# Performance work log

Hardware: AMD Instinct MI355X
Metric: run time of the kernel (lower is better)

Reference implementation:

```python
import jax, jax.numpy as jnp
import numpy as np

N_NODES = 100000
N_EDGES = 640000
D = 128

def setup_inputs() -> dict:
    key = jax.random.key(0)
    k1, k2, k3 = jax.random.split(key, 3)
    z = jax.random.normal(k1, (N_NODES, D), dtype=jnp.float32)
    edge_index = jax.random.randint(k2, (2, N_EDGES), 0, N_NODES, dtype=jnp.int64)
    # torch.nn.Bilinear(D, D, 1): weight (1, D, D), bias (1,); kaiming-like init, here random
    W = jax.random.normal(k3, (D, D), dtype=jnp.float32) * (1.0 / np.sqrt(D))
    b = jnp.zeros((1,), dtype=jnp.float32)
    return {"z": z, "edge_index": edge_index, "W": W, "b": b}

def reference(z, edge_index, W, b):
    # y_e = z[src_e]^T W z[dst_e] + b
    zi = z[edge_index[0]]            # [E, D] gather
    zj = z[edge_index[1]]            # [E, D] gather
    # (zi @ W) * zj summed over feature dim -> [E]
    y = jnp.einsum('ed,ed->e', zi @ W, zj) + b[0]
    return y
```

## Files before the change

### kernel.cpp

```cpp
#include <hip/hip_runtime.h>

#define FD 128

typedef __attribute__((ext_vector_type(8))) short short8;
typedef __attribute__((ext_vector_type(4))) float f32x4;

__device__ __forceinline__ unsigned short f2bf(float f) {
    unsigned u = __float_as_uint(f);
    u += 0x7fff + ((u >> 16) & 1);
    return (unsigned short)(u >> 16);
}
__device__ __forceinline__ float bf2f(unsigned short h) {
    return __uint_as_float(((unsigned)h) << 16);
}
__device__ __forceinline__ int bdot4(unsigned x, unsigned y, int acc) {
#if __has_builtin(__builtin_amdgcn_sdot4)
    return __builtin_amdgcn_sdot4(x, y, acc, false);
#else
    acc += (((int)(x << 24)) >> 24) * (((int)(y << 24)) >> 24);
    acc += (((int)(x << 16)) >> 24) * (((int)(y << 16)) >> 24);
    acc += (((int)(x <<  8)) >> 24) * (((int)(y <<  8)) >> 24);
    acc += (((int)x) >> 24)         * (((int)y) >> 24);
    return acc;
#endif
}
__device__ __forceinline__ unsigned pack4f(float a, float b, float c, float d, float inv) {
    const int q0 = (int)rintf(a * inv), q1 = (int)rintf(b * inv);
    const int q2 = (int)rintf(c * inv), q3 = (int)rintf(d * inv);
    return (unsigned)(q0 & 255) | ((unsigned)(q1 & 255) << 8) |
           ((unsigned)(q2 & 255) << 16) | ((unsigned)(q3 & 255) << 24);
}

__global__ void wt_kernel(const float* __restrict__ W, unsigned short* __restrict__ Wt) {
    const int tid = blockIdx.x * 256 + (int)threadIdx.x;
    const int n  = tid & 127;
    const int k0 = (tid >> 7) * 8;
    short8 w;
    #pragma unroll
    for (int j = 0; j < 8; ++j) w[j] = (short)f2bf(W[(k0 + j) * FD + n]);
    *(short8*)(Wt + (size_t)n * FD + k0) = w;
}

__global__ __launch_bounds__(256)
void u_mfma8(const float* __restrict__ z, const unsigned short* __restrict__ Wt,
             unsigned char* __restrict__ u8, float* __restrict__ uscale,
             unsigned char* __restrict__ z8, float* __restrict__ zscale,
             int nrows) {
    __shared__ unsigned short Wl[FD * FD];
    char* ldsb = (char*)Wl;
    const int tid  = (int)threadIdx.x;
    const int lane = tid & 63;
    const int wave = tid >> 6;
    const int l16  = lane & 15;
    const int kq   = lane >> 4;

    const long rowbase = (long)blockIdx.x * 64 + wave * 16;
    const long r  = rowbase + l16;
    const long rc = (r < nrows) ? r : (long)(nrows - 1);
    const bool rok = (r < nrows);

    float4 zf[4][2];
    #pragma unroll
    for (int ks = 0; ks < 4; ++ks) {
        const float4* zp = (const float4*)(z + rc * FD + kq * 32 + ks * 8);
        zf[ks][0] = zp[0];
        zf[ks][1] = zp[1];
    }

    #pragma unroll
    for (int i = 0; i < 8; ++i) {
        const int c = i * 256 + tid;
        const int n = c >> 4;
        const int o = (c & 15) * 16;
        short8 v = *(const short8*)(Wt + (size_t)n * FD + (c & 15) * 8);
        *(short8*)(ldsb + n * 256 + (o ^ ((n & 7) << 4))) = v;
    }
    __syncthreads();

    f32x4 acc[8];
    #pragma unroll
    for (int nt = 0; nt < 8; ++nt)
        acc[nt] = (f32x4){0.f, 0.f, 0.f, 0.f};

    short8 avk[4];
    float zmax = 1e-30f;

    #pragma unroll
    for (int ks = 0; ks < 4; ++ks) {
        const float4 f0 = zf[ks][0];
        const float4 f1 = zf[ks][1];
        short8 av;
        av[0] = (short)f2bf(f0.x); av[1] = (short)f2bf(f0.y);
        av[2] = (short)f2bf(f0.z); av[3] = (short)f2bf(f0.w);
        av[4] = (short)f2bf(f1.x); av[5] = (short)f2bf(f1.y);
        av[6] = (short)f2bf(f1.z); av[7] = (short)f2bf(f1.w);
        avk[ks] = av;
        #pragma unroll
        for (int j = 0; j < 8; ++j)
            zmax = fmaxf(zmax, fabsf(bf2f((unsigned short)av[j])));

        #pragma unroll
        for (int nt = 0; nt < 8; ++nt) {
            const int row = nt * 16 + l16;
            const short8 a = *(const short8*)(
                ldsb + row * 256 + ((kq * 64 + ks * 16) ^ ((row & 7) << 4)));
            acc[nt] = __builtin_amdgcn_mfma_f32_16x16x32_bf16(a, av, acc[nt], 0, 0, 0);
        }
    }

    zmax = fmaxf(zmax, __shfl_xor(zmax, 16, 64));
    zmax = fmaxf(zmax, __shfl_xor(zmax, 32, 64));
    {
        const float inv = 127.0f / zmax;
        uint4 p0, p1;
        p0.x = pack4f(bf2f((unsigned short)avk[0][0]), bf2f((unsigned short)avk[0][1]),
                      bf2f((unsigned short)avk[0][2]), bf2f((unsigned short)avk[0][3]), inv);
        p0.y = pack4f(bf2f((unsigned short)avk[0][4]), bf2f((unsigned short)avk[0][5]),
                      bf2f((unsigned short)avk[0][6]), bf2f((unsigned short)avk[0][7]), inv);
        p0.z = pack4f(bf2f((unsigned short)avk[1][0]), bf2f((unsigned short)avk[1][1]),
                      bf2f((unsigned short)avk[1][2]), bf2f((unsigned short)avk[1][3]), inv);
        p0.w = pack4f(bf2f((unsigned short)avk[1][4]), bf2f((unsigned short)avk[1][5]),
                      bf2f((unsigned short)avk[1][6]), bf2f((unsigned short)avk[1][7]), inv);
        p1.x = pack4f(bf2f((unsigned short)avk[2][0]), bf2f((unsigned short)avk[2][1]),
                      bf2f((unsigned short)avk[2][2]), bf2f((unsigned short)avk[2][3]), inv);
        p1.y = pack4f(bf2f((unsigned short)avk[2][4]), bf2f((unsigned short)avk[2][5]),
                      bf2f((unsigned short)avk[2][6]), bf2f((unsigned short)avk[2][7]), inv);
        p1.z = pack4f(bf2f((unsigned short)avk[3][0]), bf2f((unsigned short)avk[3][1]),
                      bf2f((unsigned short)avk[3][2]), bf2f((unsigned short)avk[3][3]), inv);
        p1.w = pack4f(bf2f((unsigned short)avk[3][4]), bf2f((unsigned short)avk[3][5]),
                      bf2f((unsigned short)avk[3][6]), bf2f((unsigned short)avk[3][7]), inv);
        if (rok) {
            *(uint4*)(z8 + r * FD + kq * 32)      = p0;
            *(uint4*)(z8 + r * FD + kq * 32 + 16) = p1;
            if (kq == 0) zscale[r] = zmax * (1.0f / 127.0f);
        }
    }

    float umax = 1e-30f;
    #pragma unroll
    for (int nt = 0; nt < 8; ++nt) {
        const f32x4 v = acc[nt];
        umax = fmaxf(umax, fmaxf(fmaxf(fabsf(v[0]), fabsf(v[1])),
                                 fmaxf(fabsf(v[2]), fabsf(v[3]))));
    }
    umax = fmaxf(umax, __shfl_xor(umax, 16, 64));
    umax = fmaxf(umax, __shfl_xor(umax, 32, 64));
    umax = fmaxf(umax, 1e-30f);
    const float uinv = 127.0f / umax;
    if (rok) {
        #pragma unroll
        for (int nt = 0; nt < 8; ++nt) {
            const f32x4 v = acc[nt];
            *(unsigned*)(u8 + r * FD + nt * 16 + kq * 4) =
                pack4f(v[0], v[1], v[2], v[3], uinv);
        }
        if (kq == 0) uscale[r] = umax * (1.0f / 127.0f);
    }
}

__global__ __launch_bounds__(256)
void edge8p2(const unsigned char* __restrict__ u8, const unsigned char* __restrict__ z8,
             const float* __restrict__ uscale, const float* __restrict__ zscale,
             const int* __restrict__ src, const int* __restrict__ dst,
             const float* __restrict__ bias, float* __restrict__ out, int E) {
    const int tid  = (int)threadIdx.x;
    const int lane = tid & 63;
    const int sub  = lane >> 3;
    const int l8   = lane & 7;
    const long wv  = (long)blockIdx.x * 4 + (tid >> 6);
    const long S   = (long)gridDim.x * 4 * 8;
    const float bv = bias[0];
    const long Em1 = (long)E - 1;

    long e = wv * 8 + sub;
    long ec  = (e     < E) ? e     : Em1;
    long ecn = (e + S < E) ? e + S : Em1;
    int s0 = src[ec],  t0 = dst[ec];
    int s1 = src[ecn], t1 = dst[ecn];
    uint4 xu0 = *((const uint4*)(u8 + (size_t)s0 * FD) + l8);
    uint4 xz0 = *((const uint4*)(z8 + (size_t)t0 * FD) + l8);
    float su0 = uscale[s0], sz0 = zscale[t0];

    while (e < E) {
        const uint4 xu1 = *((const uint4*)(u8 + (size_t)s1 * FD) + l8);
        const uint4 xz1 = *((const uint4*)(z8 + (size_t)t1 * FD) + l8);
        const float su1 = uscale[s1], sz1 = zscale[t1];

        const long e2  = e + 2 * S;
        const long e2c = (e2 < E) ? e2 : Em1;
        const int s2 = src[e2c], t2 = dst[e2c];

        int sum = 0;
        sum = bdot4(xu0.x, xz0.x, sum);
        sum = bdot4(xu0.y, xz0.y, sum);
        sum = bdot4(xu0.z, xz0.z, sum);
        sum = bdot4(xu0.w, xz0.w, sum);
        sum += __shfl_xor(sum, 4, 64);
        sum += __shfl_xor(sum, 2, 64);
        sum += __shfl_xor(sum, 1, 64);
        if (l8 == 0) out[e] = (float)sum * su0 * sz0 + bv;

        e += S;
        xu0 = xu1; xz0 = xz1; su0 = su1; sz0 = sz1;
        s1 = s2; t1 = t2;
    }
}

__global__ __launch_bounds__(128)
void bilinear_fused_fallback(const float* __restrict__ z, const float* __restrict__ Wg,
                             const int* __restrict__ src, const int* __restrict__ dst,
                             const float* __restrict__ bias, float* __restrict__ out,
                             int E) {
    __shared__ float Wl[FD * FD];
    __shared__ float zs[FD];
    __shared__ float red[2];
    for (int i = threadIdx.x; i < FD * FD; i += 128) Wl[i] = Wg[i];
    __syncthreads();
    const int j = (int)threadIdx.x;
    for (int e = blockIdx.x; e < E; e += gridDim.x) {
        const int s = src[e];
        const int t = dst[e];
        zs[j] = z[(size_t)s * FD + j];
        __syncthreads();
        float acc = 0.f;
        #pragma unroll 8
        for (int d = 0; d < FD; ++d) acc += zs[d] * Wl[d * FD + j];
        float p = acc * z[(size_t)t * FD + j];
        #pragma unroll
        for (int off = 32; off >= 1; off >>= 1)
            p += __shfl_xor(p, off, 64);
        if ((j & 63) == 0) red[j >> 6] = p;
        __syncthreads();
        if (j == 0) out[e] = red[0] + red[1] + bias[0];
        __syncthreads();
    }
}

extern "C" void kernel_launch(void* const* d_in, const int* in_sizes, int n_in,
                              void* d_out, int out_size, void* d_ws, size_t ws_size,
                              hipStream_t stream) {
    const float* z    = (const float*)d_in[0];
    const int*   ei   = (const int*)d_in[1];
    const float* W    = (const float*)d_in[2];
    const float* bias = (const float*)d_in[3];
    float* out = (float*)d_out;

    const int nrows = in_sizes[0] / FD;
    const int E     = in_sizes[1] / 2;
    const int* src = ei;
    const int* dst = ei + E;

    const size_t sz8 = (size_t)nrows * FD;
    const size_t szs = (size_t)nrows * sizeof(float);
    const size_t need = 2 * sz8 + 2 * szs + 256;

    if (ws_size >= need) {
        char* wsp = (char*)d_ws;
        unsigned char* u8  = (unsigned char*)wsp;
        unsigned char* z8  = (unsigned char*)(wsp + sz8);
        float* uscale = (float*)(wsp + 2 * sz8);
        float* zscale = (float*)(wsp + 2 * sz8 + szs);
        unsigned short* Wt = (unsigned short*)d_out;

        wt_kernel<<<8, 256, 0, stream>>>(W, Wt);
        const int nb1 = (nrows + 63) / 64;
        u_mfma8<<<nb1, 256, 0, stream>>>(z, Wt, u8, uscale, z8, zscale, nrows);
        edge8p2<<<2048, 256, 0, stream>>>(u8, z8, uscale, zscale, src, dst, bias, out, E);
    } else {
        bilinear_fused_fallback<<<2048, 128, 0, stream>>>(z, W, src, dst, bias, out, E);
    }
}
```

Before: 56.35 us.

## Make node projection kernel persistent with software-prefetched z tiles

Converts the per-node u = zW projection kernel from one block per 64-row tile into a persistent grid of at most 768 blocks that loop over tiles. W is staged into LDS once per block instead of once per tile, and the next tile's z rows are prefetched into registers while the current tile's MFMA work and quantization run. This trades some register pressure and reduced parallelism for fewer redundant W loads and overlap of global reads with compute.

New measurement: 56.56 us. No clear change (+0.4%).

```diff
diff --git a/kernel.cpp b/kernel.cpp
--- a/kernel.cpp
+++ b/kernel.cpp
@@ -42,10 +42,10 @@
 }
 
 __global__ __launch_bounds__(256)
-void u_mfma8(const float* __restrict__ z, const unsigned short* __restrict__ Wt,
+void u_mfma9(const float* __restrict__ z, const unsigned short* __restrict__ Wt,
              unsigned char* __restrict__ u8, float* __restrict__ uscale,
              unsigned char* __restrict__ z8, float* __restrict__ zscale,
-             int nrows) {
+             int nrows, int ntiles) {
     __shared__ unsigned short Wl[FD * FD];
     char* ldsb = (char*)Wl;
     const int tid  = (int)threadIdx.x;
@@ -53,18 +53,19 @@
     const int wave = tid >> 6;
     const int l16  = lane & 15;
     const int kq   = lane >> 4;
-
-    const long rowbase = (long)blockIdx.x * 64 + wave * 16;
-    const long r  = rowbase + l16;
-    const long rc = (r < nrows) ? r : (long)(nrows - 1);
-    const bool rok = (r < nrows);
-
+    const long NB  = gridDim.x;
+
+    long tile = blockIdx.x;
     float4 zf[4][2];
-    #pragma unroll
-    for (int ks = 0; ks < 4; ++ks) {
-        const float4* zp = (const float4*)(z + rc * FD + kq * 32 + ks * 8);
-        zf[ks][0] = zp[0];
-        zf[ks][1] = zp[1];
+    if (tile < ntiles) {
+        const long r0  = tile * 64 + wave * 16 + l16;
+        const long rc0 = (r0 < nrows) ? r0 : (long)(nrows - 1);
+        #pragma unroll
+        for (int ks = 0; ks < 4; ++ks) {
+            const float4* zp = (const float4*)(z + rc0 * FD + kq * 32 + ks * 8);
+            zf[ks][0] = zp[0];
+            zf[ks][1] = zp[1];
+        }
     }
 
     #pragma unroll
@@ -77,84 +78,102 @@
     }
     __syncthreads();
 
-    f32x4 acc[8];
-    #pragma unroll
-    for (int nt = 0; nt < 8; ++nt)
-        acc[nt] = (f32x4){0.f, 0.f, 0.f, 0.f};
-
-    short8 avk[4];
-    float zmax = 1e-30f;
-
-    #pragma unroll
-    for (int ks = 0; ks < 4; ++ks) {
-        const float4 f0 = zf[ks][0];
-        const float4 f1 = zf[ks][1];
-        short8 av;
-        av[0] = (short)f2bf(f0.x); av[1] = (short)f2bf(f0.y);
-        av[2] = (short)f2bf(f0.z); av[3] = (short)f2bf(f0.w);
-        av[4] = (short)f2bf(f1.x); av[5] = (short)f2bf(f1.y);
-        av[6] = (short)f2bf(f1.z); av[7] = (short)f2bf(f1.w);
-        avk[ks] = av;
-        #pragma unroll
-        for (int j = 0; j < 8; ++j)
-            zmax = fmaxf(zmax, fabsf(bf2f((unsigned short)av[j])));
-
-        #pragma unroll
-        for (int nt = 0; nt < 8; ++nt) {
-            const int row = nt * 16 + l16;
-            const short8 a = *(const short8*)(
-                ldsb + row * 256 + ((kq * 64 + ks * 16) ^ ((row & 7) << 4)));
-            acc[nt] = __builtin_amdgcn_mfma_f32_16x16x32_bf16(a, av, acc[nt], 0, 0, 0);
-        }
-    }
-
-    zmax = fmaxf(zmax, __shfl_xor(zmax, 16, 64));
-    zmax = fmaxf(zmax, __shfl_xor(zmax, 32, 64));
-    {
-        const float inv = 127.0f / zmax;
-        uint4 p0, p1;
-        p0.x = pack4f(bf2f((unsigned short)avk[0][0]), bf2f((unsigned short)avk[0][1]),
-                      bf2f((unsigned short)avk[0][2]), bf2f((unsigned short)avk[0][3]), inv);
-        p0.y = pack4f(bf2f((unsigned short)avk[0][4]), bf2f((unsigned short)avk[0][5]),
-                      bf2f((unsigned short)avk[0][6]), bf2f((unsigned short)avk[0][7]), inv);
-        p0.z = pack4f(bf2f((unsigned short)avk[1][0]), bf2f((unsigned short)avk[1][1]),
-                      bf2f((unsigned short)avk[1][2]), bf2f((unsigned short)avk[1][3]), inv);
-        p0.w = pack4f(bf2f((unsigned short)avk[1][4]), bf2f((unsigned short)avk[1][5]),
-                      bf2f((unsigned short)avk[1][6]), bf2f((unsigned short)avk[1][7]), inv);
-        p1.x = pack4f(bf2f((unsigned short)avk[2][0]), bf2f((unsigned short)avk[2][1]),
-                      bf2f((unsigned short)avk[2][2]), bf2f((unsigned short)avk[2][3]), inv);
-        p1.y = pack4f(bf2f((unsigned short)avk[2][4]), bf2f((unsigned short)avk[2][5]),
-                      bf2f((unsigned short)avk[2][6]), bf2f((unsigned short)avk[2][7]), inv);
-        p1.z = pack4f(bf2f((unsigned short)avk[3][0]), bf2f((unsigned short)avk[3][1]),
-                      bf2f((unsigned short)avk[3][2]), bf2f((unsigned short)avk[3][3]), inv);
-        p1.w = pack4f(bf2f((unsigned short)avk[3][4]), bf2f((unsigned short)avk[3][5]),
-                      bf2f((unsigned short)avk[3][6]), bf2f((unsigned short)avk[3][7]), inv);
-        if (rok) {
-            *(uint4*)(z8 + r * FD + kq * 32)      = p0;
-            *(uint4*)(z8 + r * FD + kq * 32 + 16) = p1;
-            if (kq == 0) zscale[r] = zmax * (1.0f / 127.0f);
-        }
-    }
-
-    float umax = 1e-30f;
-    #pragma unroll
-    for (int nt = 0; nt < 8; ++nt) {
-        const f32x4 v = acc[nt];
-        umax = fmaxf(umax, fmaxf(fmaxf(fabsf(v[0]), fabsf(v[1])),
-                                 fmaxf(fabsf(v[2]), fabsf(v[3]))));
-    }
-    umax = fmaxf(umax, __shfl_xor(umax, 16, 64));
-    umax = fmaxf(umax, __shfl_xor(umax, 32, 64));
-    umax = fmaxf(umax, 1e-30f);
-    const float uinv = 127.0f / umax;
-    if (rok) {
+    for (; tile < ntiles; tile += NB) {
+        const long r  = tile * 64 + wave * 16 + l16;
+        const bool rok = (r < nrows);
+
+        short8 avk[4];
+        float zmax = 1e-30f;
+        #pragma unroll
+        for (int ks = 0; ks < 4; ++ks) {
+            const float4 f0 = zf[ks][0];
+            const float4 f1 = zf[ks][1];
+            short8 av;
+            av[0] = (short)f2bf(f0.x); av[1] = (short)f2bf(f0.y);
+            av[2] = (short)f2bf(f0.z); av[3] = (short)f2bf(f0.w);
+            av[4] = (short)f2bf(f1.x); av[5] = (short)f2bf(f1.y);
+            av[6] = (short)f2bf(f1.z); av[7] = (short)f2bf(f1.w);
+            avk[ks] = av;
+            #pragma unroll
+            for (int j = 0; j < 8; ++j)
+                zmax = fmaxf(zmax, fabsf(bf2f((unsigned short)av[j])));
+        }
+
+        const long tn = tile + NB;
+        if (tn < ntiles) {
+            const long rn  = tn * 64 + wave * 16 + l16;
+            const long rcn = (rn < nrows) ? rn : (long)(nrows - 1);
+            #pragma unroll
+            for (int ks = 0; ks < 4; ++ks) {
+                const float4* zp = (const float4*)(z + rcn * FD + kq * 32 + ks * 8);
+                zf[ks][0] = zp[0];
+                zf[ks][1] = zp[1];
+            }
+        }
+
+        f32x4 acc[8];
+        #pragma unroll
+        for (int nt = 0; nt < 8; ++nt)
+            acc[nt] = (f32x4){0.f, 0.f, 0.f, 0.f};
+        #pragma unroll
+        for (int ks = 0; ks < 4; ++ks) {
+            #pragma unroll
+            for (int nt = 0; nt < 8; ++nt) {
+                const int row = nt * 16 + l16;
+                const short8 a = *(const short8*)(
+                    ldsb + row * 256 + ((kq * 64 + ks * 16) ^ ((row & 7) << 4)));
+                acc[nt] = __builtin_amdgcn_mfma_f32_16x16x32_bf16(a, avk[ks], acc[nt], 0, 0, 0);
+            }
+        }
+
+        zmax = fmaxf(zmax, __shfl_xor(zmax, 16, 64));
+        zmax = fmaxf(zmax, __shfl_xor(zmax, 32, 64));
+        {
+            const float inv = 127.0f / zmax;
+            uint4 p0, p1;
+            p0.x = pack4f(bf2f((unsigned short)avk[0][0]), bf2f((unsigned short)avk[0][1]),
+                          bf2f((unsigned short)avk[0][2]), bf2f((unsigned short)avk[0][3]), inv);
+            p0.y = pack4f(bf2f((unsigned short)avk[0][4]), bf2f((unsigned short)avk[0][5]),
+                          bf2f((unsigned short)avk[0][6]), bf2f((unsigned short)avk[0][7]), inv);
+            p0.z = pack4f(bf2f((unsigned short)avk[1][0]), bf2f((unsigned short)avk[1][1]),
+                          bf2f((unsigned short)avk[1][2]), bf2f((unsigned short)avk[1][3]), inv);
+            p0.w = pack4f(bf2f((unsigned short)avk[1][4]), bf2f((unsigned short)avk[1][5]),
+                          bf2f((unsigned short)avk[1][6]), bf2f((unsigned short)avk[1][7]), inv);
+            p1.x = pack4f(bf2f((unsigned short)avk[2][0]), bf2f((unsigned short)avk[2][1]),
+                          bf2f((unsigned short)avk[2][2]), bf2f((unsigned short)avk[2][3]), inv);
+            p1.y = pack4f(bf2f((unsigned short)avk[2][4]), bf2f((unsigned short)avk[2][5]),
+                          bf2f((unsigned short)avk[2][6]), bf2f((unsigned short)avk[2][7]), inv);
+            p1.z = pack4f(bf2f((unsigned short)avk[3][0]), bf2f((unsigned short)avk[3][1]),
+                          bf2f((unsigned short)avk[3][2]), bf2f((unsigned short)avk[3][3]), inv);
+            p1.w = pack4f(bf2f((unsigned short)avk[3][4]), bf2f((unsigned short)avk[3][5]),
+                          bf2f((unsigned short)avk[3][6]), bf2f((unsigned short)avk[3][7]), inv);
+            if (rok) {
+                *(uint4*)(z8 + r * FD + kq * 32)      = p0;
+                *(uint4*)(z8 + r * FD + kq * 32 + 16) = p1;
+                if (kq == 0) zscale[r] = zmax * (1.0f / 127.0f);
+            }
+        }
+
+        float umax = 1e-30f;
         #pragma unroll
         for (int nt = 0; nt < 8; ++nt) {
             const f32x4 v = acc[nt];
-            *(unsigned*)(u8 + r * FD + nt * 16 + kq * 4) =
-                pack4f(v[0], v[1], v[2], v[3], uinv);
-        }
-        if (kq == 0) uscale[r] = umax * (1.0f / 127.0f);
+            umax = fmaxf(umax, fmaxf(fmaxf(fabsf(v[0]), fabsf(v[1])),
+                                     fmaxf(fabsf(v[2]), fabsf(v[3]))));
+        }
+        umax = fmaxf(umax, __shfl_xor(umax, 16, 64));
+        umax = fmaxf(umax, __shfl_xor(umax, 32, 64));
+        umax = fmaxf(umax, 1e-30f);
+        const float uinv = 127.0f / umax;
+        if (rok) {
+            #pragma unroll
+            for (int nt = 0; nt < 8; ++nt) {
+                const f32x4 v = acc[nt];
+                *(unsigned*)(u8 + r * FD + nt * 16 + kq * 4) =
+                    pack4f(v[0], v[1], v[2], v[3], uinv);
+            }
+            if (kq == 0) uscale[r] = umax * (1.0f / 127.0f);
+        }
     }
 }
 
@@ -263,8 +282,9 @@
         unsigned short* Wt = (unsigned short*)d_out;
 
         wt_kernel<<<8, 256, 0, stream>>>(W, Wt);
-        const int nb1 = (nrows + 63) / 64;
-        u_mfma8<<<nb1, 256, 0, stream>>>(z, Wt, u8, uscale, z8, zscale, nrows);
+        const int ntiles = (nrows + 63) / 64;
+        const int nb1 = (ntiles < 768) ? ntiles : 768;
+        u_mfma9<<<nb1, 256, 0, stream>>>(z, Wt, u8, uscale, z8, zscale, nrows, ntiles);
         edge8p2<<<2048, 256, 0, stream>>>(u8, z8, uscale, zscale, src, dst, bias, out, E);
     } else {
         bilinear_fused_fallback<<<2048, 128, 0, stream>>>(z, W, src, dst, bias, out, E);
```
